# Performance work log

Hardware: AMD Instinct MI355X
Metric: run time of the kernel (lower is better)

## Reference

```python
import jax, jax.numpy as jnp
import numpy as np

T = 32        # time_step
H = 64        # n_hidden (and dense width)
A = 8         # nb_actions
OBS_DIM = 512
B = 4096      # sequences; obs rows = B*T
LN_EPS = 1e-12  # tf.contrib.layers.layer_norm epsilon


def setup_inputs() -> dict:
    key = jax.random.key(0)
    ks = jax.random.split(key, 10)
    s = 0.1
    return {
        "obs":  jax.random.normal(ks[0], (B * T, OBS_DIM), jnp.float32),
        "W0":   jax.random.normal(ks[1], (OBS_DIM, H), jnp.float32) * s,
        "b0":   jnp.zeros((H,), jnp.float32),
        "gamma": jnp.ones((H,), jnp.float32),
        "beta":  jnp.zeros((H,), jnp.float32),
        "Wfw":  jax.random.normal(ks[2], (2 * H, 4 * H), jnp.float32) * s,
        "bfw":  jnp.zeros((4 * H,), jnp.float32),
        "Wbw":  jax.random.normal(ks[3], (2 * H, 4 * H), jnp.float32) * s,
        "bbw":  jnp.zeros((4 * H,), jnp.float32),
        "Wc":   jax.random.uniform(ks[4], (H, A), jnp.float32, -0.003, 0.003),
        "bc":   jnp.zeros((A,), jnp.float32),
    }


def _lstm_scan(xs, W, b):
    """BasicLSTMCell (forget_bias=1.0). xs: [T, B, H] -> hs: [T, B, H]."""
    nb = xs.shape[1]
    init = (jnp.zeros((nb, H), xs.dtype), jnp.zeros((nb, H), xs.dtype))

    def step(carry, x_t):
        c, h = carry
        z = jnp.concatenate([x_t, h], axis=-1) @ W + b  # [B, 4H]
        i, j, f, o = jnp.split(z, 4, axis=-1)           # TF gate order i,j,f,o
        c = c * jax.nn.sigmoid(f + 1.0) + jax.nn.sigmoid(i) * jnp.tanh(j)
        h = jnp.tanh(c) * jax.nn.sigmoid(o)
        return (c, h), h

    _, hs = jax.lax.scan(step, init, xs)
    return hs


def reference(obs, W0, b0, gamma, beta, Wfw, bfw, Wbw, bbw, Wc, bc):
    # dense(64) + layer_norm + relu
    x = obs @ W0 + b0                                   # [B*T, H]
    mu = jnp.mean(x, axis=-1, keepdims=True)
    var = jnp.mean(jnp.square(x - mu), axis=-1, keepdims=True)
    x = gamma * (x - mu) / jnp.sqrt(var + LN_EPS) + beta
    x = jax.nn.relu(x)

    xt = x.reshape(-1, T, H).transpose(1, 0, 2)          # [T, B, H]
    hs_fw = _lstm_scan(xt, Wfw, bfw)                     # [T, B, H]
    hs_bw = _lstm_scan(xt[::-1], Wbw, bbw)[::-1]         # reverse-in, reverse-out

    # tf.reshape on the (fw, bw) tuple stacks along a new leading axis:
    # [2, B, T, H] -> [2B, T*H, 1]; conv1d(kernel=stride=H) == per-step proj.
    y = jnp.stack([hs_fw.transpose(1, 0, 2), hs_bw.transpose(1, 0, 2)], axis=0)
    y = y.reshape(-1, T, H)                              # [2B, T, H]
    out = jnp.tanh(jnp.einsum('btk,ka->bta', y, Wc) + bc)  # [2B, T, A]
    return out
```

## Files before the change

kernel.cpp:

```cpp
#include <hip/hip_runtime.h>

typedef __attribute__((ext_vector_type(8))) short bf16x8;
typedef __attribute__((ext_vector_type(4))) float f32x4;

#define MFMA_BF16 __builtin_amdgcn_mfma_f32_16x16x32_bf16

__device__ __forceinline__ unsigned short f2bf(float f) {
  union { float f; unsigned u; } v; v.f = f;
  unsigned r = v.u + 0x7FFFu + ((v.u >> 16) & 1u);
  return (unsigned short)(r >> 16);
}
__device__ __forceinline__ float sigm(float x) {
  return __builtin_amdgcn_rcpf(1.f + __expf(-x));
}
__device__ __forceinline__ float tanh_f(float x) {
  return 1.f - 2.f * __builtin_amdgcn_rcpf(1.f + __expf(2.f * x));
}

__global__ void k0_conv(const float* __restrict__ W0, const float* __restrict__ Wfw,
                        const float* __restrict__ Wbw, unsigned short* __restrict__ wfrag,
                        unsigned short* __restrict__ wlstm) {
  int gid = blockIdx.x * 256 + threadIdx.x;
  if (gid < 4096) {
    int f = gid >> 6, l = gid & 63;
    int k0 = (f >> 2) * 32 + ((l >> 4) << 3);
    int n = (f & 3) * 16 + (l & 15);
    bf16x8 v;
#pragma unroll
    for (int j = 0; j < 8; ++j) v[j] = (short)f2bf(W0[(k0 + j) * 64 + n]);
    *(bf16x8*)(wfrag + gid * 8) = v;
  } else if (gid < 12288) {
    int g2 = gid - 4096;
    const float* W = (g2 < 4096) ? Wfw : Wbw;
    int f = (g2 & 4095) >> 6, l = g2 & 63;
    int wv = f >> 4, gate = (f >> 2) & 3, kf = f & 3;
    int col = gate * 64 + wv * 16 + (l & 15);
    int kr = kf * 32 + ((l >> 4) << 3);
    bf16x8 v;
#pragma unroll
    for (int j = 0; j < 8; ++j) v[j] = (short)f2bf(W[(kr + j) * 256 + col]);
    *(bf16x8*)(wlstm + g2 * 8) = v;
  }
}

__global__ __launch_bounds__(256, 2) void k_dense_ln(
    const float* __restrict__ obs, const unsigned short* __restrict__ wfrag,
    const float* __restrict__ b0, const float* __restrict__ gam,
    const float* __restrict__ bet, unsigned short* __restrict__ xout) {
  __shared__ unsigned short xs[4096];
  const int tid = threadIdx.x, w = tid >> 6, l = tid & 63;
  const int g = l >> 4, c = l & 15;
  const long rb = (long)blockIdx.x * 64 + w * 16;

  float b0v[4], gv[4], bv[4];
#pragma unroll
  for (int nt = 0; nt < 4; ++nt) {
    int col = nt * 16 + c;
    b0v[nt] = b0[col]; gv[nt] = gam[col]; bv[nt] = bet[col];
  }

  const float* arow = obs + (rb + c) * 512 + g * 8;
  const unsigned short* wfl = wfrag + l * 8;

  f32x4 acc[4];
#pragma unroll
  for (int nt = 0; nt < 4; ++nt) acc[nt] = (f32x4){0.f, 0.f, 0.f, 0.f};

  float4 a0 = *(const float4*)(arow);
  float4 a1 = *(const float4*)(arow + 4);
  bf16x8 Bc[4];
#pragma unroll
  for (int nt = 0; nt < 4; ++nt) Bc[nt] = *(const bf16x8*)(wfl + nt * 512);

#pragma unroll
  for (int kf = 0; kf < 16; ++kf) {
    bf16x8 af;
    af[0] = (short)f2bf(a0.x); af[1] = (short)f2bf(a0.y);
    af[2] = (short)f2bf(a0.z); af[3] = (short)f2bf(a0.w);
    af[4] = (short)f2bf(a1.x); af[5] = (short)f2bf(a1.y);
    af[6] = (short)f2bf(a1.z); af[7] = (short)f2bf(a1.w);
    float4 n0, n1;
    bf16x8 Bn[4];
    if (kf < 15) {
      n0 = *(const float4*)(arow + (kf + 1) * 32);
      n1 = *(const float4*)(arow + (kf + 1) * 32 + 4);
#pragma unroll
      for (int nt = 0; nt < 4; ++nt)
        Bn[nt] = *(const bf16x8*)(wfl + ((kf + 1) * 4 + nt) * 512);
    }
#pragma unroll
    for (int nt = 0; nt < 4; ++nt)
      acc[nt] = MFMA_BF16(af, Bc[nt], acc[nt], 0, 0, 0);
    if (kf < 15) {
      a0 = n0; a1 = n1;
#pragma unroll
      for (int nt = 0; nt < 4; ++nt) Bc[nt] = Bn[nt];
    }
  }

  float vv[4][4], s1[4], s2[4];
#pragma unroll
  for (int r = 0; r < 4; ++r) { s1[r] = 0.f; s2[r] = 0.f; }
#pragma unroll
  for (int nt = 0; nt < 4; ++nt)
#pragma unroll
    for (int r = 0; r < 4; ++r) {
      float val = acc[nt][r] + b0v[nt];
      vv[nt][r] = val; s1[r] += val; s2[r] += val * val;
    }
#pragma unroll
  for (int r = 0; r < 4; ++r) {
#pragma unroll
    for (int m = 1; m <= 8; m <<= 1) {
      s1[r] += __shfl_xor(s1[r], m);
      s2[r] += __shfl_xor(s2[r], m);
    }
  }
  unsigned short* xw = xs + w * 1024;
#pragma unroll
  for (int r = 0; r < 4; ++r) {
    float mu = s1[r] * 0.015625f;
    float var = s2[r] * 0.015625f - mu * mu;
    float inv = rsqrtf(var + 1e-12f);
    int row = g * 4 + r;
#pragma unroll
    for (int nt = 0; nt < 4; ++nt) {
      float xn = (vv[nt][r] - mu) * inv * gv[nt] + bv[nt];
      xw[(row * 64 + nt * 16 + c) ^ (g << 3)] = f2bf(fmaxf(xn, 0.f));
    }
  }
#pragma unroll
  for (int m2 = 0; m2 < 2; ++m2) {
    int m = m2 * 64 + l;
    int row = m >> 3, u8 = m & 7;
    bf16x8 v = *(const bf16x8*)(xw + ((row * 64 + u8 * 8) ^ ((row >> 2) << 3)));
    *(bf16x8*)(xout + (rb + row) * 64 + u8 * 8) = v;
  }
}

__global__ __launch_bounds__(256, 2) void k_lstm(
    const unsigned short* __restrict__ x, const unsigned short* __restrict__ wlstm,
    const float* __restrict__ bfw, const float* __restrict__ bbw,
    const float* __restrict__ Wc, const float* __restrict__ bc,
    float* __restrict__ out) {
  __shared__ unsigned short xl[64 * 64 * 8];
  __shared__ unsigned short hl[2 * 2 * 64 * 8];
  const int tid = threadIdx.x, w = tid >> 6, l = tid & 63;
  const int g = l >> 4, c = l & 15;
  const int dir = blockIdx.x >> 8;
  const int sq = (blockIdx.x & 255) * 16;
  const float* bias = dir ? bbw : bfw;

  bf16x8 Bf[4][4];
  const unsigned short* wl = wlstm + ((long)dir * 4096 + w * 16 * 64) * 8;
#pragma unroll
  for (int gate = 0; gate < 4; ++gate)
#pragma unroll
    for (int kf = 0; kf < 4; ++kf)
      Bf[gate][kf] = *(const bf16x8*)(wl + ((gate * 4 + kf) * 64 + l) * 8);
  float bz[4];
#pragma unroll
  for (int gate = 0; gate < 4; ++gate) bz[gate] = bias[gate * 64 + w * 16 + c];

  bf16x8 Pc[2];
#pragma unroll
  for (int kf = 0; kf < 2; ++kf)
#pragma unroll
    for (int j = 0; j < 8; ++j) Pc[kf][j] = 0;
  float bcv = 0.f;
  if (w == 0 && c < 8) {
#pragma unroll
    for (int kf = 0; kf < 2; ++kf)
#pragma unroll
      for (int j = 0; j < 8; ++j)
        Pc[kf][j] = (short)f2bf(Wc[(kf * 32 + g * 8 + j) * 8 + c]);
    bcv = bc[c];
  }

  const unsigned short* xg = x + (long)sq * 2048;
  for (int q = tid; q < 4096; q += 256) {
    bf16x8 v = *(const bf16x8*)(xg + q * 8);
    int s = q >> 8, te = (q >> 3) & 31, u0 = q & 7;
    int fidx = te * 2 + (u0 >> 2);
    int dl = ((u0 & 3) * 16 + s) ^ (fidx & 7);
    *(bf16x8*)(xl + (fidx * 64 + dl) * 8) = v;
  }
  for (int i = tid; i < 512; i += 256) ((unsigned*)hl)[i] = 0u;
  float cs[4] = {0.f, 0.f, 0.f, 0.f};
  __syncthreads();

  const int hq = w >> 1;
  const int hgp = ((w & 1) * 2 + (c >> 3)) * 16;
  const int hlo = c & 7;

  int p = 0;
  for (int t = 0; t < 32; ++t) {
    const int te = dir ? 31 - t : t;
    const int f0 = te * 2, f1 = te * 2 + 1;
    bf16x8 Ax0 = *(const bf16x8*)(xl + (f0 * 64 + (l ^ (f0 & 7))) * 8);
    bf16x8 Ax1 = *(const bf16x8*)(xl + (f1 * 64 + (l ^ (f1 & 7))) * 8);
    bf16x8 Ah0 = *(const bf16x8*)(hl + p * 1024 + l * 8);
    bf16x8 Ah1 = *(const bf16x8*)(hl + p * 1024 + (64 + l) * 8);

    f32x4 acc[4];
#pragma unroll
    for (int gate = 0; gate < 4; ++gate)
      acc[gate] = (f32x4){bz[gate], bz[gate], bz[gate], bz[gate]};
#pragma unroll
    for (int gate = 0; gate < 4; ++gate) {
      acc[gate] = MFMA_BF16(Ax0, Bf[gate][0], acc[gate], 0, 0, 0);
      acc[gate] = MFMA_BF16(Ax1, Bf[gate][1], acc[gate], 0, 0, 0);
      acc[gate] = MFMA_BF16(Ah0, Bf[gate][2], acc[gate], 0, 0, 0);
      acc[gate] = MFMA_BF16(Ah1, Bf[gate][3], acc[gate], 0, 0, 0);
    }

    const int wb = (p ^ 1) * 1024;
#pragma unroll
    for (int r = 0; r < 4; ++r) {
      float si = sigm(acc[0][r]);
      float tj = tanh_f(acc[1][r]);
      float sf = sigm(acc[2][r] + 1.f);
      float so = sigm(acc[3][r]);
      cs[r] = cs[r] * sf + si * tj;
      hl[wb + (hq * 64 + hgp + 4 * g + r) * 8 + hlo] = f2bf(tanh_f(cs[r]) * so);
    }
    __syncthreads();

    if (w == 0) {
      bf16x8 Ph0 = *(const bf16x8*)(hl + wb + l * 8);
      bf16x8 Ph1 = *(const bf16x8*)(hl + wb + (64 + l) * 8);
      f32x4 pa = (f32x4){0.f, 0.f, 0.f, 0.f};
      pa = MFMA_BF16(Ph0, Pc[0], pa, 0, 0, 0);
      pa = MFMA_BF16(Ph1, Pc[1], pa, 0, 0, 0);
      if (c < 8) {
#pragma unroll
        for (int r = 0; r < 4; ++r) {
          long orow = (long)dir * 4096 + sq + 4 * g + r;
          out[(orow * 32 + te) * 8 + c] = tanh_f(pa[r] + bcv);
        }
      }
    }
    p ^= 1;
  }
}

extern "C" void kernel_launch(void* const* d_in, const int* in_sizes, int n_in,
                              void* d_out, int out_size, void* d_ws, size_t ws_size,
                              hipStream_t stream) {
  const float* obs = (const float*)d_in[0];
  const float* W0  = (const float*)d_in[1];
  const float* b0  = (const float*)d_in[2];
  const float* gam = (const float*)d_in[3];
  const float* bet = (const float*)d_in[4];
  const float* Wfw = (const float*)d_in[5];
  const float* bfw = (const float*)d_in[6];
  const float* Wbw = (const float*)d_in[7];
  const float* bbw = (const float*)d_in[8];
  const float* Wc  = (const float*)d_in[9];
  const float* bc  = (const float*)d_in[10];
  float* out = (float*)d_out;

  unsigned short* wfrag = (unsigned short*)d_ws;
  unsigned short* wlstm = wfrag + 4096 * 8;
  unsigned short* xbf   = wlstm + 8192 * 8;

  k0_conv<<<48, 256, 0, stream>>>(W0, Wfw, Wbw, wfrag, wlstm);
  k_dense_ln<<<2048, 256, 0, stream>>>(obs, wfrag, b0, gam, bet, xbf);
  k_lstm<<<512, 256, 0, stream>>>(xbf, wlstm, bfw, bbw, Wc, bc, out);
}
```

Before: 111.7 us.

## Stream LSTM inputs via ring buffer prefetch, reuse h fragments for projection, use hw bf16 convert

The LSTM kernel no longer stages the whole 64KB per-block input sequence in LDS up front. It keeps a 4-slot ring buffer and prefetches the timestep two steps ahead from global memory during each step, which shrinks LDS use and should allow higher occupancy. The output projection for step t-1 now reuses the h fragments already loaded for step t, so the separate LDS reread goes away, and an epilogue after the loop handles the last step. The float-to-bf16 conversions now use the HIP hardware and packed intrinsics. The cost is per-step global loads sitting on the recurrent critical path and more complex indexing.

Measured after the change: 106.0 us. -5.1%, faster.

```diff
diff --git a/kernel.cpp b/kernel.cpp
--- a/kernel.cpp
+++ b/kernel.cpp
@@ -1,14 +1,18 @@
 #include <hip/hip_runtime.h>
+#include <hip/hip_bf16.h>
 
 typedef __attribute__((ext_vector_type(8))) short bf16x8;
 typedef __attribute__((ext_vector_type(4))) float f32x4;
 
 #define MFMA_BF16 __builtin_amdgcn_mfma_f32_16x16x32_bf16
 
-__device__ __forceinline__ unsigned short f2bf(float f) {
-  union { float f; unsigned u; } v; v.f = f;
-  unsigned r = v.u + 0x7FFFu + ((v.u >> 16) & 1u);
-  return (unsigned short)(r >> 16);
+__device__ __forceinline__ unsigned pk2(float a, float b) {
+  __hip_bfloat162 t = __float22bfloat162_rn(make_float2(a, b));
+  return *reinterpret_cast<unsigned*>(&t);
+}
+__device__ __forceinline__ unsigned short f2bf_hw(float f) {
+  __hip_bfloat16 h = __float2bfloat16(f);
+  return *reinterpret_cast<unsigned short*>(&h);
 }
 __device__ __forceinline__ float sigm(float x) {
   return __builtin_amdgcn_rcpf(1.f + __expf(-x));
@@ -27,7 +31,7 @@
     int n = (f & 3) * 16 + (l & 15);
     bf16x8 v;
 #pragma unroll
-    for (int j = 0; j < 8; ++j) v[j] = (short)f2bf(W0[(k0 + j) * 64 + n]);
+    for (int j = 0; j < 8; ++j) v[j] = (short)f2bf_hw(W0[(k0 + j) * 64 + n]);
     *(bf16x8*)(wfrag + gid * 8) = v;
   } else if (gid < 12288) {
     int g2 = gid - 4096;
@@ -38,7 +42,7 @@
     int kr = kf * 32 + ((l >> 4) << 3);
     bf16x8 v;
 #pragma unroll
-    for (int j = 0; j < 8; ++j) v[j] = (short)f2bf(W[(kr + j) * 256 + col]);
+    for (int j = 0; j < 8; ++j) v[j] = (short)f2bf_hw(W[(kr + j) * 256 + col]);
     *(bf16x8*)(wlstm + g2 * 8) = v;
   }
 }
@@ -74,11 +78,9 @@
 
 #pragma unroll
   for (int kf = 0; kf < 16; ++kf) {
-    bf16x8 af;
-    af[0] = (short)f2bf(a0.x); af[1] = (short)f2bf(a0.y);
-    af[2] = (short)f2bf(a0.z); af[3] = (short)f2bf(a0.w);
-    af[4] = (short)f2bf(a1.x); af[5] = (short)f2bf(a1.y);
-    af[6] = (short)f2bf(a1.z); af[7] = (short)f2bf(a1.w);
+    union { bf16x8 v; unsigned u[4]; } af;
+    af.u[0] = pk2(a0.x, a0.y); af.u[1] = pk2(a0.z, a0.w);
+    af.u[2] = pk2(a1.x, a1.y); af.u[3] = pk2(a1.z, a1.w);
     float4 n0, n1;
     bf16x8 Bn[4];
     if (kf < 15) {
@@ -90,7 +92,7 @@
     }
 #pragma unroll
     for (int nt = 0; nt < 4; ++nt)
-      acc[nt] = MFMA_BF16(af, Bc[nt], acc[nt], 0, 0, 0);
+      acc[nt] = MFMA_BF16(af.v, Bc[nt], acc[nt], 0, 0, 0);
     if (kf < 15) {
       a0 = n0; a1 = n1;
 #pragma unroll
@@ -126,7 +128,7 @@
 #pragma unroll
     for (int nt = 0; nt < 4; ++nt) {
       float xn = (vv[nt][r] - mu) * inv * gv[nt] + bv[nt];
-      xw[(row * 64 + nt * 16 + c) ^ (g << 3)] = f2bf(fmaxf(xn, 0.f));
+      xw[(row * 64 + nt * 16 + c) ^ (g << 3)] = f2bf_hw(fmaxf(xn, 0.f));
     }
   }
 #pragma unroll
@@ -143,8 +145,8 @@
     const float* __restrict__ bfw, const float* __restrict__ bbw,
     const float* __restrict__ Wc, const float* __restrict__ bc,
     float* __restrict__ out) {
-  __shared__ unsigned short xl[64 * 64 * 8];
-  __shared__ unsigned short hl[2 * 2 * 64 * 8];
+  __shared__ unsigned short xr[4 * 1024];
+  __shared__ unsigned short hl[2 * 1024];
   const int tid = threadIdx.x, w = tid >> 6, l = tid & 63;
   const int g = l >> 4, c = l & 15;
   const int dir = blockIdx.x >> 8;
@@ -173,17 +175,21 @@
     for (int kf = 0; kf < 2; ++kf)
 #pragma unroll
       for (int j = 0; j < 8; ++j)
-        Pc[kf][j] = (short)f2bf(Wc[(kf * 32 + g * 8 + j) * 8 + c]);
+        Pc[kf][j] = (short)f2bf_hw(Wc[(kf * 32 + g * 8 + j) * 8 + c]);
     bcv = bc[c];
   }
 
-  const unsigned short* xg = x + (long)sq * 2048;
-  for (int q = tid; q < 4096; q += 256) {
-    bf16x8 v = *(const bf16x8*)(xg + q * 8);
-    int s = q >> 8, te = (q >> 3) & 31, u0 = q & 7;
-    int fidx = te * 2 + (u0 >> 2);
-    int dl = ((u0 & 3) * 16 + s) ^ (fidx & 7);
-    *(bf16x8*)(xl + (fidx * 64 + dl) * 8) = v;
+  const int sRow = tid >> 4, uc = tid & 15;
+  const unsigned short* xg = x + ((long)(sq + sRow) * 32) * 64 + uc * 4;
+  const unsigned xdst = ((unsigned)(((uc >> 3) * 64 + ((uc >> 1) & 3) * 16 + sRow) * 16 +
+                                    (uc & 1) * 8));
+
+  {
+    int te0 = dir ? 31 : 0, te1 = dir ? 30 : 1;
+    uint2 v0 = *(const uint2*)(xg + te0 * 64);
+    uint2 v1 = *(const uint2*)(xg + te1 * 64);
+    *(uint2*)((char*)xr + 0 * 2048 + xdst) = v0;
+    *(uint2*)((char*)xr + 1 * 2048 + xdst) = v1;
   }
   for (int i = tid; i < 512; i += 256) ((unsigned*)hl)[i] = 0u;
   float cs[4] = {0.f, 0.f, 0.f, 0.f};
@@ -196,11 +202,18 @@
   int p = 0;
   for (int t = 0; t < 32; ++t) {
     const int te = dir ? 31 - t : t;
-    const int f0 = te * 2, f1 = te * 2 + 1;
-    bf16x8 Ax0 = *(const bf16x8*)(xl + (f0 * 64 + (l ^ (f0 & 7))) * 8);
-    bf16x8 Ax1 = *(const bf16x8*)(xl + (f1 * 64 + (l ^ (f1 & 7))) * 8);
-    bf16x8 Ah0 = *(const bf16x8*)(hl + p * 1024 + l * 8);
-    bf16x8 Ah1 = *(const bf16x8*)(hl + p * 1024 + (64 + l) * 8);
+    uint2 pf;
+    const bool do_pf = (t + 2 < 32);
+    if (do_pf) {
+      int tep = dir ? 29 - t : t + 2;
+      pf = *(const uint2*)(xg + tep * 64);
+    }
+
+    const char* xs = (const char*)xr + (t & 3) * 2048;
+    bf16x8 Ax0 = *(const bf16x8*)(xs + l * 16);
+    bf16x8 Ax1 = *(const bf16x8*)(xs + 1024 + l * 16);
+    bf16x8 Ah0 = *(const bf16x8*)((const char*)hl + p * 2048 + l * 16);
+    bf16x8 Ah1 = *(const bf16x8*)((const char*)hl + p * 2048 + 1024 + l * 16);
 
     f32x4 acc[4];
 #pragma unroll
@@ -222,25 +235,41 @@
       float sf = sigm(acc[2][r] + 1.f);
       float so = sigm(acc[3][r]);
       cs[r] = cs[r] * sf + si * tj;
-      hl[wb + (hq * 64 + hgp + 4 * g + r) * 8 + hlo] = f2bf(tanh_f(cs[r]) * so);
-    }
+      hl[wb + (hq * 64 + hgp + 4 * g + r) * 8 + hlo] = f2bf_hw(tanh_f(cs[r]) * so);
+    }
+    if (do_pf) *(uint2*)((char*)xr + ((t + 2) & 3) * 2048 + xdst) = pf;
     __syncthreads();
 
-    if (w == 0) {
-      bf16x8 Ph0 = *(const bf16x8*)(hl + wb + l * 8);
-      bf16x8 Ph1 = *(const bf16x8*)(hl + wb + (64 + l) * 8);
+    if (w == 0 && t >= 1) {
       f32x4 pa = (f32x4){0.f, 0.f, 0.f, 0.f};
-      pa = MFMA_BF16(Ph0, Pc[0], pa, 0, 0, 0);
-      pa = MFMA_BF16(Ph1, Pc[1], pa, 0, 0, 0);
+      pa = MFMA_BF16(Ah0, Pc[0], pa, 0, 0, 0);
+      pa = MFMA_BF16(Ah1, Pc[1], pa, 0, 0, 0);
       if (c < 8) {
+        int tp = dir ? 32 - t : t - 1;
 #pragma unroll
         for (int r = 0; r < 4; ++r) {
           long orow = (long)dir * 4096 + sq + 4 * g + r;
-          out[(orow * 32 + te) * 8 + c] = tanh_f(pa[r] + bcv);
+          out[(orow * 32 + tp) * 8 + c] = tanh_f(pa[r] + bcv);
         }
       }
     }
     p ^= 1;
+  }
+
+  if (w == 0) {
+    bf16x8 Ph0 = *(const bf16x8*)((const char*)hl + p * 2048 + l * 16);
+    bf16x8 Ph1 = *(const bf16x8*)((const char*)hl + p * 2048 + 1024 + l * 16);
+    f32x4 pa = (f32x4){0.f, 0.f, 0.f, 0.f};
+    pa = MFMA_BF16(Ph0, Pc[0], pa, 0, 0, 0);
+    pa = MFMA_BF16(Ph1, Pc[1], pa, 0, 0, 0);
+    if (c < 8) {
+      int tp = dir ? 0 : 31;
+#pragma unroll
+      for (int r = 0; r < 4; ++r) {
+        long orow = (long)dir * 4096 + sq + 4 * g + r;
+        out[(orow * 32 + tp) * 8 + c] = tanh_f(pa[r] + bcv);
+      }
+    }
   }
 }
 
```
